# Kernel optimization log

Measured on AMD Instinct MI355X. Metric: run time of the kernel, lower is better.

The kernel has to match this reference:

```python
import jax, jax.numpy as jnp
import numpy as np

DIM = 4096
N_HEADS = 32
N_KV_HEADS = 8
HEAD_DIM = 128
ROPE_BASE = 10000.0
B, L = 4, 1024
NEG_INF = -1e9


def rope_traditional(x, base=ROPE_BASE, offset=0):
    # x: [B, H, L, Dh]; rotates interleaved pairs (x[...,2i], x[...,2i+1])
    Dh = x.shape[-1]
    Lx = x.shape[2]
    inv_freq = base ** (-jnp.arange(0, Dh, 2, dtype=jnp.float32) / Dh)  # [Dh/2]
    pos = jnp.arange(offset, offset + Lx, dtype=jnp.float32)
    ang = pos[:, None] * inv_freq  # [L, Dh/2]
    cos, sin = jnp.cos(ang), jnp.sin(ang)
    x1, x2 = x[..., ::2], x[..., 1::2]
    r1 = x1 * cos - x2 * sin
    r2 = x1 * sin + x2 * cos
    return jnp.stack([r1, r2], axis=-1).reshape(x.shape).astype(x.dtype)


def setup_inputs() -> dict:
    key = jax.random.key(0)
    ks = jax.random.split(key, 5)
    x = jax.random.normal(ks[0], (B, L, DIM), dtype=jnp.float32)
    # additive causal mask: 0 on/below diag, -inf-like above
    mask = jnp.where(jnp.tril(jnp.ones((L, L), dtype=bool)), 0.0, NEG_INF).astype(jnp.float32)
    wq = jax.random.normal(ks[1], (DIM, N_HEADS * HEAD_DIM), dtype=jnp.float32) * 0.02
    wk = jax.random.normal(ks[2], (DIM, N_KV_HEADS * HEAD_DIM), dtype=jnp.float32) * 0.02
    wv = jax.random.normal(ks[3], (DIM, N_KV_HEADS * HEAD_DIM), dtype=jnp.float32) * 0.02
    wo = jax.random.normal(ks[4], (N_HEADS * HEAD_DIM, DIM), dtype=jnp.float32) * 0.02
    return {"x": x, "mask": mask, "wq": wq, "wk": wk, "wv": wv, "wo": wo}


def reference(x, mask, wq, wk, wv, wo):
    Bx, Lx, D = x.shape
    scale = HEAD_DIM ** -0.5
    repeats = N_HEADS // N_KV_HEADS
    q = (x @ wq).reshape(Bx, Lx, N_HEADS, HEAD_DIM).transpose(0, 2, 1, 3)      # [B,H,L,Dh]
    k = (x @ wk).reshape(Bx, Lx, N_KV_HEADS, HEAD_DIM).transpose(0, 2, 1, 3)   # [B,Hkv,L,Dh]
    v = (x @ wv).reshape(Bx, Lx, N_KV_HEADS, HEAD_DIM).transpose(0, 2, 1, 3)
    # GQA expansion: head h attends to kv head h % n_kv_heads (matches
    # expand_dims+repeat(axis=1)+reshape in the original)
    k = jnp.tile(k, (1, repeats, 1, 1))  # [B,H,L,Dh]
    v = jnp.tile(v, (1, repeats, 1, 1))
    # cache=None path: rope with offset 0
    q = rope_traditional(q)
    k = rope_traditional(k)
    scores = jnp.einsum("bhqd,bhkd->bhqk", q * scale, k) + mask
    probs = jax.nn.softmax(scores.astype(jnp.float32), axis=-1).astype(scores.dtype)
    out = jnp.einsum("bhqk,bhkd->bhqd", probs, v)
    out = out.transpose(0, 2, 1, 3).reshape(Bx, Lx, D)
    return out @ wo
```

## Files before the change

kernel.cpp:

```cpp
#include <hip/hip_runtime.h>
#include <stdint.h>

typedef unsigned short u16;
typedef __bf16 bf16x8 __attribute__((ext_vector_type(8)));
typedef float f32x4 __attribute__((ext_vector_type(4)));

__device__ __forceinline__ u16 f2b(float x) {
  uint32_t b = __float_as_uint(x);
  b += 0x7fff + ((b >> 16) & 1);
  return (u16)(b >> 16);
}
__device__ __forceinline__ float b2f(u16 u) {
  return __uint_as_float(((uint32_t)u) << 16);
}

#define GLD16(src, dst)                                                                  \
  __builtin_amdgcn_global_load_lds((const __attribute__((address_space(1))) void*)(src),\
                                   (__attribute__((address_space(3))) void*)(dst), 16, 0, 0)

__device__ __forceinline__ f32x4 mfma16(bf16x8 a, bf16x8 b, f32x4 c) {
  return __builtin_amdgcn_mfma_f32_16x16x32_bf16(a, b, c, 0, 0, 0);
}

__global__ void k_rope_table(float2* __restrict__ tab) {
  int i = blockIdx.x * 256 + threadIdx.x;
  int l = i >> 6, d = i & 63;
  float inv = powf(10000.0f, -(float)(2 * d) / 128.0f);
  float ang = (float)l * inv;
  float s, c;
  sincosf(ang, &s, &c);
  tab[i] = make_float2(c, s);
}

__global__ void k_cast8(const float* __restrict__ src, u16* __restrict__ dst) {
  size_t i = (size_t)blockIdx.x * 256 + threadIdx.x;
  const float4* s4 = (const float4*)src;
  float4 a = s4[2 * i], b = s4[2 * i + 1];
  union { u16 u[8]; uint4 v; } o;
  o.u[0] = f2b(a.x); o.u[1] = f2b(a.y); o.u[2] = f2b(a.z); o.u[3] = f2b(a.w);
  o.u[4] = f2b(b.x); o.u[5] = f2b(b.y); o.u[6] = f2b(b.z); o.u[7] = f2b(b.w);
  ((uint4*)dst)[i] = o.v;
}

__global__ __launch_bounds__(256) void k_tcast(const float* __restrict__ src,
                                               u16* __restrict__ dst, int R, int C) {
  __shared__ u16 t[64][72];
  int tiles_c = C >> 6;
  int tr = blockIdx.x / tiles_c, tc = blockIdx.x % tiles_c;
  int tid = threadIdx.x;
  {
    int rr = tid >> 4, cv = tid & 15;
#pragma unroll
    for (int it = 0; it < 4; ++it) {
      int row = rr + it * 16;
      float4 v = *(const float4*)(src + (size_t)(tr * 64 + row) * C + tc * 64 + cv * 4);
      t[row][cv * 4 + 0] = f2b(v.x);
      t[row][cv * 4 + 1] = f2b(v.y);
      t[row][cv * 4 + 2] = f2b(v.z);
      t[row][cv * 4 + 3] = f2b(v.w);
    }
  }
  __syncthreads();
  {
    int cc = tid >> 3, g = tid & 7;
#pragma unroll
    for (int it = 0; it < 2; ++it) {
      int c = cc + it * 32;
      union { u16 u[8]; uint4 v; } o;
#pragma unroll
      for (int j = 0; j < 8; ++j) o.u[j] = t[g * 8 + j][c];
      *(uint4*)(dst + (size_t)(tc * 64 + c) * R + tr * 64 + g * 8) = o.v;
    }
  }
}

__global__ __launch_bounds__(256) void k_vtrans(const u16* __restrict__ qkv,
                                                u16* __restrict__ vrt) {
  __shared__ u16 t[64][72];
  int b = blockIdx.x >> 8;
  int tt = blockIdx.x & 255;
  int tr = tt >> 4, tc = tt & 15;
  int tid = threadIdx.x;
  {
    int rr = tid >> 3, g = tid & 7;
#pragma unroll
    for (int it = 0; it < 2; ++it) {
      int row = rr + it * 32;
      union { u16 u[8]; uint4 v; } o;
      o.v = *(const uint4*)(qkv + (size_t)(b * 1024 + tr * 64 + row) * 6144 + 5120 + tc * 64 + g * 8);
#pragma unroll
      for (int j = 0; j < 8; ++j) t[row][g * 8 + j] = o.u[j];
    }
  }
  __syncthreads();
  {
    int cc = tid >> 3, g = tid & 7;
#pragma unroll
    for (int it = 0; it < 2; ++it) {
      int c = cc + it * 32;
      union { u16 u[8]; uint4 v; } o;
#pragma unroll
      for (int j = 0; j < 8; ++j) o.u[j] = t[g * 8 + j][c];
      *(uint4*)(vrt + (size_t)(b * 1024 + tc * 64 + c) * 1024 + tr * 64 + g * 8) = o.v;
    }
  }
}

__global__ __launch_bounds__(320) void k_rope8(const u16* __restrict__ qkv,
                                               const float2* __restrict__ tab,
                                               u16* __restrict__ qr, u16* __restrict__ kr) {
  int row = blockIdx.x;
  int j = threadIdx.x * 8;
  int b = row >> 10, l = row & 1023;
  const float qs = 0.12751586584003446f;
  bool isq = (j < 2048);
  int jj = isq ? j : (j - 2048);
  int h = jj >> 6, dp = jj & 63;
  const u16* src = qkv + (size_t)row * 6144 + (isq ? 0 : 4096) + h * 128 + 2 * dp;
  uint4 v0 = *(const uint4*)(src);
  uint4 v1 = *(const uint4*)(src + 8);
  const float2* tb = tab + l * 64 + dp;
  float sc = isq ? qs : 1.0f;
  union { u16 u[16]; uint4 v[2]; } o;
  const uint32_t* w = (const uint32_t*)&v0;
#pragma unroll
  for (int i = 0; i < 8; ++i) {
    uint32_t pair = (i < 4) ? w[i] : ((const uint32_t*)&v1)[i - 4];
    float2 cs = tb[i];
    float x1 = b2f((u16)pair), x2 = b2f((u16)(pair >> 16));
    float r1 = (x1 * cs.x - x2 * cs.y) * sc;
    float r2 = (x1 * cs.y + x2 * cs.x) * sc;
    o.u[2 * i] = f2b(r1);
    o.u[2 * i + 1] = f2b(r2);
  }
  u16* dst = isq ? (qr + ((size_t)((b * 32 + h) * 1024 + l)) * 128 + 2 * dp)
                 : (kr + ((size_t)((b * 8 + h) * 1024 + l)) * 128 + 2 * dp);
  *(uint4*)(dst) = o.v[0];
  *(uint4*)(dst + 8) = o.v[1];
}

#define STAGE2(s0, s1, koff, ldsoff)          \
  GLD16((s0) + (koff), dst0 + (ldsoff));      \
  GLD16((s1) + (koff), dst1 + (ldsoff));

#define LOADB(base, kh)                                                   \
  bfr[0] = *(const bf16x8*)((base) + (kh) * 8192 + 0 * 512);              \
  bfr[1] = *(const bf16x8*)((base) + (kh) * 8192 + 1 * 512);              \
  bfr[2] = *(const bf16x8*)((base) + (kh) * 8192 + 2 * 512);              \
  bfr[3] = *(const bf16x8*)((base) + (kh) * 8192 + 3 * 512);

#define LOADA(base, kh, mh)                                               \
  afr[0] = *(const bf16x8*)((base) + (kh) * 8192 + (mh) * 2048 + 0 * 512);\
  afr[1] = *(const bf16x8*)((base) + (kh) * 8192 + (mh) * 2048 + 1 * 512);\
  afr[2] = *(const bf16x8*)((base) + (kh) * 8192 + (mh) * 2048 + 2 * 512);\
  afr[3] = *(const bf16x8*)((base) + (kh) * 8192 + (mh) * 2048 + 3 * 512);

#define PH(mh)                                                            \
  __builtin_amdgcn_s_barrier();                                           \
  asm volatile("s_waitcnt lgkmcnt(0)" ::: "memory");                      \
  __builtin_amdgcn_s_setprio(1);                                          \
  _Pragma("unroll") for (int mm = 0; mm < 4; ++mm)                        \
    _Pragma("unroll") for (int n_ = 0; n_ < 4; ++n_)                      \
      acc[(mh) * 4 + mm][n_] = mfma16(afr[mm], bfr[n_], acc[(mh) * 4 + mm][n_]); \
  __builtin_amdgcn_s_setprio(0);                                          \
  __builtin_amdgcn_s_barrier();

#define PHV(mh, n)                                                        \
  __builtin_amdgcn_s_barrier();                                           \
  asm volatile("s_waitcnt lgkmcnt(0)" ::: "memory");                      \
  __builtin_amdgcn_s_setprio(1);                                          \
  _Pragma("unroll") for (int mm = 0; mm < 4; ++mm)                        \
    _Pragma("unroll") for (int n_ = 0; n_ < 4; ++n_)                      \
      acc[(mh) * 4 + mm][n_] = mfma16(afr[mm], bfr[n_], acc[(mh) * 4 + mm][n_]); \
  __builtin_amdgcn_s_setprio(0);                                          \
  asm volatile("s_waitcnt vmcnt(" #n ")" ::: "memory");                   \
  __builtin_amdgcn_s_barrier();

#define VMC(n) asm volatile("s_waitcnt vmcnt(" #n ")" ::: "memory");

template <typename OutT>
__global__ __launch_bounds__(512, 2) void k_gemm8(const u16* __restrict__ A,
                                                  const u16* __restrict__ Bt,
                                                  OutT* __restrict__ C,
                                                  int M, int N, int K) {
  extern __shared__ u16 lds[];
  const int tid = threadIdx.x;
  const int lane = tid & 63, wid = tid >> 6;
  const int l16 = lane & 15, lhi = lane >> 4;
  const int wm = wid >> 2, wn = wid & 3;

  const int nbn = N >> 8;
  int bid = blockIdx.x;
  const int cpx = gridDim.x >> 3;
  bid = (bid & 7) * cpx + (bid >> 3);
  const int bm = (bid / nbn) << 8;
  const int bn = (bid % nbn) << 8;

  const u16* Ag = A + (size_t)bm * K;
  const u16* Bg = Bt + (size_t)bn * K;

  const int swz = (lhi ^ ((l16 >> 1) & 3)) << 3;
  const u16* pA0 = lds + wm * 4096 + l16 * 32 + swz;
  const u16* pA1 = pA0 + 32768;
  const u16* pB0 = lds + 16384 + wn * 2048 + l16 * 32 + swz;
  const u16* pB1 = pB0 + 32768;

  const int r0 = tid >> 2, g0 = tid & 3;
  const int r1 = r0 + 128;
  const size_t so0 = (size_t)r0 * K + ((g0 ^ ((r0 >> 1) & 3)) << 3);
  const size_t so1 = (size_t)r1 * K + ((g0 ^ ((r1 >> 1) & 3)) << 3);
  const u16* sA0 = Ag + so0;
  const u16* sA1 = Ag + so1;
  const u16* sB0 = Bg + so0;
  const u16* sB1 = Bg + so1;
  u16* dst0 = lds + wid * 512;
  u16* dst1 = lds + 4096 + wid * 512;

  f32x4 acc[8][4] = {};
  bf16x8 bfr[4], afr[4];

  STAGE2(sA0, sA1, 0, 0);
  STAGE2(sA0, sA1, 32, 8192);
  STAGE2(sB0, sB1, 0, 16384);
  STAGE2(sB0, sB1, 32, 24576);
  STAGE2(sB0, sB1, 64, 49152);
  STAGE2(sA0, sA1, 64, 32768);
  STAGE2(sB0, sB1, 96, 57344);
  VMC(6)
  __builtin_amdgcn_s_barrier();

  const int nt = K >> 6;
  for (int t = 0; t < nt - 2; t += 2) {
    const int kA1 = (t + 1) * 64 + 32;
    const int k2 = (t + 2) * 64;
    const int k3 = (t + 3) * 64;
    LOADB(pB0, 0)
    LOADA(pA0, 0, 0)
    STAGE2(sA0, sA1, kA1, 40960);
    PH(0)
    LOADA(pA0, 0, 1)
    STAGE2(sB0, sB1, k2, 16384);
    PH(1)
    LOADB(pB0, 1)
    LOADA(pA0, 1, 0)
    STAGE2(sA0, sA1, k2, 0);
    PH(0)
    LOADA(pA0, 1, 1)
    STAGE2(sB0, sB1, k2 + 32, 24576);
    PHV(1, 6)
    LOADB(pB1, 0)
    LOADA(pA1, 0, 0)
    STAGE2(sA0, sA1, k2 + 32, 8192);
    PH(0)
    LOADA(pA1, 0, 1)
    STAGE2(sB0, sB1, k3, 49152);
    PH(1)
    LOADB(pB1, 1)
    LOADA(pA1, 1, 0)
    STAGE2(sA0, sA1, k3, 32768);
    PH(0)
    LOADA(pA1, 1, 1)
    STAGE2(sB0, sB1, k3 + 32, 57344);
    PHV(1, 6)
  }
  {
    const int kA1 = (nt - 1) * 64 + 32;
    LOADB(pB0, 0)
    LOADA(pA0, 0, 0)
    STAGE2(sA0, sA1, kA1, 40960);
    PH(0)
    LOADA(pA0, 0, 1)
    PH(1)
    LOADB(pB0, 1)
    LOADA(pA0, 1, 0)
    PH(0)
    LOADA(pA0, 1, 1)
    PHV(1, 0)
    LOADB(pB1, 0)
    LOADA(pA1, 0, 0)
    PH(0)
    LOADA(pA1, 0, 1)
    PH(1)
    LOADB(pB1, 1)
    LOADA(pA1, 1, 0)
    PH(0)
    LOADA(pA1, 1, 1)
    PH(1)
  }

#pragma unroll
  for (int m = 0; m < 8; ++m) {
    int row = bm + wm * 128 + m * 16 + lhi * 4;
#pragma unroll
    for (int n = 0; n < 4; ++n) {
      int col = bn + wn * 64 + n * 16 + l16;
#pragma unroll
      for (int r = 0; r < 4; ++r) {
        float v = acc[m][n][r];
        size_t idx = (size_t)(row + r) * N + col;
        if constexpr (sizeof(OutT) == 2) C[idx] = f2b(v);
        else C[idx] = v;
      }
    }
  }
}

__global__ __launch_bounds__(512) void k_attn(const u16* __restrict__ qr,
                                              const u16* __restrict__ kr,
                                              const u16* __restrict__ vrt,
                                              u16* __restrict__ ao) {
  __shared__ u16 Klds[8192];
  __shared__ u16 Vlds[8192];
  __shared__ u16 Plds[9216];
  int bid = blockIdx.x;
  int qb = bid & 7, h = (bid >> 3) & 31, b = bid >> 8;
  int kvh = h & 7;
  int lane = threadIdx.x & 63, w = threadIdx.x >> 6;
  int l16 = lane & 15, lhi = lane >> 4;
  int qmin = qb * 128 + w * 16;

  const u16* qbase = qr + ((size_t)((b * 32 + h) * 1024) + qmin + l16) * 128;
  bf16x8 aq[4];
#pragma unroll
  for (int kc = 0; kc < 4; ++kc) aq[kc] = *(const bf16x8*)(qbase + kc * 32 + lhi * 8);

  const u16* Kg = kr + (size_t)(b * 8 + kvh) * (1024 * 128);
  const u16* Vg = vrt + (size_t)(b * 8 + kvh) * (128 * 1024);

  float m_run[4] = {-1e30f, -1e30f, -1e30f, -1e30f};
  float l_part[4] = {0.f, 0.f, 0.f, 0.f};
  f32x4 o[8] = {};

  int nkb = 2 * qb + 2;
  for (int kb = 0; kb < nkb; ++kb) {
    int kv0 = kb * 64;
#pragma unroll
    for (int i = 0; i < 2; ++i) {
      int c = w * 128 + i * 64 + lane;
      int krow = c >> 4, g = c & 15;
      GLD16(Kg + (size_t)(kv0 + krow) * 128 + ((g ^ (krow & 7)) * 8),
            Klds + (w * 128 + i * 64) * 8);
    }
#pragma unroll
    for (int i = 0; i < 2; ++i) {
      int c = w * 128 + i * 64 + lane;
      int d = c >> 3, g = c & 7;
      GLD16(Vg + (size_t)d * 1024 + kv0 + ((g ^ (d & 7)) * 8),
            Vlds + (w * 128 + i * 64) * 8);
    }
    __syncthreads();

    f32x4 s[4] = {};
#pragma unroll
    for (int kc = 0; kc < 4; ++kc) {
#pragma unroll
      for (int n = 0; n < 4; ++n) {
        int kv = n * 16 + l16;
        int g = kc * 4 + lhi;
        bf16x8 bk = *(const bf16x8*)(Klds + kv * 128 + ((g ^ (kv & 7)) * 8));
        s[n] = mfma16(aq[kc], bk, s[n]);
      }
    }
    if (kv0 + 63 > qmin) {
#pragma unroll
      for (int n = 0; n < 4; ++n)
#pragma unroll
        for (int r = 0; r < 4; ++r) {
          int q = qmin + lhi * 4 + r;
          int kv = kv0 + n * 16 + l16;
          if (kv > q) s[n][r] = -1e30f;
        }
    }
    float mx[4];
    bool need = false;
#pragma unroll
    for (int r = 0; r < 4; ++r) {
      float m0 = fmaxf(fmaxf(s[0][r], s[1][r]), fmaxf(s[2][r], s[3][r]));
      m0 = fmaxf(m0, __shfl_xor(m0, 1));
      m0 = fmaxf(m0, __shfl_xor(m0, 2));
      m0 = fmaxf(m0, __shfl_xor(m0, 4));
      m0 = fmaxf(m0, __shfl_xor(m0, 8));
      mx[r] = m0;
      need = need || (m0 > m_run[r] + 11.0f);
    }
    if (__any(need)) {
#pragma unroll
      for (int r = 0; r < 4; ++r) {
        float mn = fmaxf(m_run[r], mx[r]);
        float sf = exp2f(m_run[r] - mn);
        m_run[r] = mn;
        l_part[r] *= sf;
#pragma unroll
        for (int nd = 0; nd < 8; ++nd) o[nd][r] *= sf;
      }
    }
    u16* pw = Plds + w * 1152;
#pragma unroll
    for (int r = 0; r < 4; ++r) {
      float lsum = 0.f;
#pragma unroll
      for (int n = 0; n < 4; ++n) {
        float p = exp2f(s[n][r] - m_run[r]);
        lsum += p;
        pw[(lhi * 4 + r) * 72 + n * 16 + l16] = f2b(p);
      }
      l_part[r] += lsum;
    }
#pragma unroll
    for (int kc = 0; kc < 2; ++kc) {
      bf16x8 ap = *(const bf16x8*)(pw + l16 * 72 + kc * 32 + lhi * 8);
#pragma unroll
      for (int nd = 0; nd < 8; ++nd) {
        int d = nd * 16 + l16;
        int g = kc * 4 + lhi;
        bf16x8 bv = *(const bf16x8*)(Vlds + d * 64 + ((g ^ (d & 7)) * 8));
        o[nd] = mfma16(ap, bv, o[nd]);
      }
    }
    __syncthreads();
  }
#pragma unroll
  for (int r = 0; r < 4; ++r) {
    float l = l_part[r];
    l += __shfl_xor(l, 1);
    l += __shfl_xor(l, 2);
    l += __shfl_xor(l, 4);
    l += __shfl_xor(l, 8);
    float inv = 1.0f / l;
    int q = qmin + lhi * 4 + r;
    u16* orow = ao + ((size_t)(b * 1024 + q)) * 4096 + h * 128;
#pragma unroll
    for (int nd = 0; nd < 8; ++nd) orow[nd * 16 + l16] = f2b(o[nd][r] * inv);
  }
}

extern "C" void kernel_launch(void* const* d_in, const int* in_sizes, int n_in,
                              void* d_out, int out_size, void* d_ws, size_t ws_size,
                              hipStream_t stream) {
  const float* x = (const float*)d_in[0];
  const float* wq = (const float*)d_in[2];
  const float* wk = (const float*)d_in[3];
  const float* wv = (const float*)d_in[4];
  const float* wo = (const float*)d_in[5];

  char* ws = (char*)d_ws;
  u16* xb = (u16*)(ws + 0);
  u16* wcat = (u16*)(ws + 33554432);
  u16* qr = (u16*)(ws + 0);
  u16* kr = (u16*)(ws + 33554432);
  u16* vrt = (u16*)(ws + 41943040);
  u16* ao = (u16*)(ws + 50331648);
  u16* wob = (u16*)(ws + 83886080);
  float2* tab = (float2*)(ws + 117440512);
  u16* qkv = (u16*)d_out;

  hipFuncSetAttribute((const void*)k_gemm8<u16>,
                      hipFuncAttributeMaxDynamicSharedMemorySize, 131072);
  hipFuncSetAttribute((const void*)k_gemm8<float>,
                      hipFuncAttributeMaxDynamicSharedMemorySize, 131072);

  k_rope_table<<<256, 256, 0, stream>>>(tab);
  k_cast8<<<8192, 256, 0, stream>>>(x, xb);
  k_tcast<<<4096, 256, 0, stream>>>(wq, wcat, 4096, 4096);
  k_tcast<<<1024, 256, 0, stream>>>(wk, wcat + (size_t)4096 * 4096, 4096, 1024);
  k_tcast<<<1024, 256, 0, stream>>>(wv, wcat + (size_t)5120 * 4096, 4096, 1024);
  k_tcast<<<4096, 256, 0, stream>>>(wo, wob, 4096, 4096);
  k_gemm8<u16><<<384, 512, 131072, stream>>>(xb, wcat, qkv, 4096, 6144, 4096);
  k_rope8<<<4096, 320, 0, stream>>>(qkv, tab, qr, kr);
  k_vtrans<<<1024, 256, 0, stream>>>(qkv, vrt);
  k_attn<<<1024, 512, 0, stream>>>(qr, kr, vrt, ao);
  k_gemm8<float><<<256, 512, 131072, stream>>>(ao, wob, (float*)d_out, 4096, 4096, 4096);
}
```

Baseline: 539.6 us.

## Prefetch next K/V tile into registers to overlap loads with compute

Replaces the direct global-to-LDS loads of K and V tiles with register prefetching: the next tile is loaded into registers at the start of each iteration, while the current tile's QK and PV MFMAs run, then written to LDS between two barriers. This is meant to hide global memory latency behind compute instead of stalling at the barrier after each tile load. It costs extra VGPRs, which may reduce occupancy, and adds a second barrier per iteration.

```diff
diff --git a/kernel.cpp b/kernel.cpp
--- a/kernel.cpp
+++ b/kernel.cpp
@@ -327,28 +327,42 @@
   const u16* Kg = kr + (size_t)(b * 8 + kvh) * (1024 * 128);
   const u16* Vg = vrt + (size_t)(b * 8 + kvh) * (128 * 1024);
 
+  const int c0 = w * 128 + lane;
+  const int c1 = c0 + 64;
+  const int kr0 = c0 >> 4, kg0 = c0 & 15;
+  const int kr1 = c1 >> 4, kg1 = c1 & 15;
+  const int ks0 = (kg0 ^ (kr0 & 7)) * 8;
+  const int ks1 = (kg1 ^ (kr1 & 7)) * 8;
+  const int vd0 = c0 >> 3, vg0 = c0 & 7;
+  const int vd1 = c1 >> 3, vg1 = c1 & 7;
+  const int vs0 = (vg0 ^ (vd0 & 7)) * 8;
+  const int vs1 = (vg1 ^ (vd1 & 7)) * 8;
+
+  uint4 kreg0, kreg1, vreg0, vreg1;
+#define LOADKV(kv0_)                                                          \
+  kreg0 = *(const uint4*)(Kg + (size_t)((kv0_) + kr0) * 128 + ks0);           \
+  kreg1 = *(const uint4*)(Kg + (size_t)((kv0_) + kr1) * 128 + ks1);           \
+  vreg0 = *(const uint4*)(Vg + (size_t)vd0 * 1024 + (kv0_) + vs0);            \
+  vreg1 = *(const uint4*)(Vg + (size_t)vd1 * 1024 + (kv0_) + vs1);
+#define WRITEKV()                                                             \
+  *(uint4*)(Klds + c0 * 8) = kreg0;                                           \
+  *(uint4*)(Klds + c1 * 8) = kreg1;                                           \
+  *(uint4*)(Vlds + c0 * 8) = vreg0;                                           \
+  *(uint4*)(Vlds + c1 * 8) = vreg1;
+
   float m_run[4] = {-1e30f, -1e30f, -1e30f, -1e30f};
   float l_part[4] = {0.f, 0.f, 0.f, 0.f};
   f32x4 o[8] = {};
 
   int nkb = 2 * qb + 2;
+  LOADKV(0)
+  WRITEKV()
+  __syncthreads();
+
   for (int kb = 0; kb < nkb; ++kb) {
     int kv0 = kb * 64;
-#pragma unroll
-    for (int i = 0; i < 2; ++i) {
-      int c = w * 128 + i * 64 + lane;
-      int krow = c >> 4, g = c & 15;
-      GLD16(Kg + (size_t)(kv0 + krow) * 128 + ((g ^ (krow & 7)) * 8),
-            Klds + (w * 128 + i * 64) * 8);
-    }
-#pragma unroll
-    for (int i = 0; i < 2; ++i) {
-      int c = w * 128 + i * 64 + lane;
-      int d = c >> 3, g = c & 7;
-      GLD16(Vg + (size_t)d * 1024 + kv0 + ((g ^ (d & 7)) * 8),
-            Vlds + (w * 128 + i * 64) * 8);
-    }
-    __syncthreads();
+    const bool more = (kb + 1) < nkb;
+    if (more) { LOADKV(kv0 + 64) }
 
     f32x4 s[4] = {};
 #pragma unroll
@@ -417,7 +431,12 @@
         o[nd] = mfma16(ap, bv, o[nd]);
       }
     }
-    __syncthreads();
+    __builtin_amdgcn_s_barrier();
+    if (more) {
+      WRITEKV()
+      asm volatile("s_waitcnt lgkmcnt(0)" ::: "memory");
+    }
+    __builtin_amdgcn_s_barrier();
   }
 #pragma unroll
   for (int r = 0; r < 4; ++r) {
@@ -432,6 +451,8 @@
 #pragma unroll
     for (int nd = 0; nd < 8; ++nd) orow[nd * 16 + l16] = f2b(o[nd][r] * inv);
   }
+#undef LOADKV
+#undef WRITEKV
 }
 
 extern "C" void kernel_launch(void* const* d_in, const int* in_sizes, int n_in,
```

After: 563.1 us. +4.3%, slower.
